# Performance work log

Hardware: AMD Instinct MI355X
Metric: run time of the kernel (lower is better)

The kernel has to match this reference:

```python
import jax, jax.numpy as jnp
import numpy as np
import math

D_MODEL = 1024
NUM_HEADS = 16
B, L = 2, 2048
# scale_level=0, patch_time_span=1 -> effective_stride=1
PERIODS = (1.0, 30.0)
WEIGHTS = (0.8, 0.4)
SIGMAS = (0.5, 2.0)


def setup_inputs() -> dict:
    key = jax.random.key(0)
    ks = jax.random.split(key, 10)
    s = 1.0 / math.sqrt(D_MODEL)
    inp = {
        "x": jax.random.normal(ks[0], (B, L, D_MODEL), dtype=jnp.float32),
        "Wq": jax.random.normal(ks[1], (D_MODEL, D_MODEL), dtype=jnp.float32) * s,
        "bq": jax.random.normal(ks[2], (D_MODEL,), dtype=jnp.float32) * 0.01,
        "Wk": jax.random.normal(ks[3], (D_MODEL, D_MODEL), dtype=jnp.float32) * s,
        "bk": jax.random.normal(ks[4], (D_MODEL,), dtype=jnp.float32) * 0.01,
        "Wv": jax.random.normal(ks[5], (D_MODEL, D_MODEL), dtype=jnp.float32) * s,
        "bv": jax.random.normal(ks[6], (D_MODEL,), dtype=jnp.float32) * 0.01,
        "Wo": jax.random.normal(ks[7], (D_MODEL, D_MODEL), dtype=jnp.float32) * s,
        "bo": jax.random.normal(ks[8], (D_MODEL,), dtype=jnp.float32) * 0.01,
        "prior_lambda": jnp.asarray(2.0, dtype=jnp.float32),
    }
    return inp


def _gaussian_mask(length):
    idx = jnp.arange(length, dtype=jnp.float32)
    delta = jnp.abs(idx[:, None] - idx[None, :])  # [L, L]
    mask = jnp.zeros_like(delta)
    for p, w, sigma in zip(PERIODS, WEIGHTS, SIGMAS):
        if p < 0.2:
            continue
        mask = mask + w * jnp.exp(-((delta - p) ** 2) / (2.0 * sigma ** 2))
    return mask


def reference(x, Wq, bq, Wk, bk, Wv, bv, Wo, bo, prior_lambda):
    Bx, Lx, D = x.shape
    H = NUM_HEADS
    hd = D // H

    def split_heads(t):  # [B, L, D] -> [B, H, L, hd]
        return t.reshape(Bx, Lx, H, hd).transpose(0, 2, 1, 3)

    Q = split_heads(x @ Wq.T + bq)
    K = split_heads(x @ Wk.T + bk)
    V = split_heads(x @ Wv.T + bv)

    scores = jnp.einsum("bhqd,bhkd->bhqk", Q, K) / math.sqrt(hd)
    scores = scores + prior_lambda * _gaussian_mask(Lx)[None, None, :, :]
    attn = jax.nn.softmax(scores, axis=-1)
    out = jnp.einsum("bhqk,bhkd->bhqd", attn, V)
    out = out.transpose(0, 2, 1, 3).reshape(Bx, Lx, D)
    return out @ Wo.T + bo
```

## Files before the change

### kernel.cpp

```cpp
#include <hip/hip_runtime.h>

#define D_MODEL 1024
#define SEQ_L   2048
#define NHEADS  16
#define HDIM    64
#define NROWS   4096

#define QSCALE 0.18033688011112042f
#define LOG2E  1.4426950408889634f

#if __has_builtin(__builtin_amdgcn_exp2f)
#define EXP2F(x) __builtin_amdgcn_exp2f(x)
#else
#define EXP2F(x) __expf((x) * 0.6931471805599453f)
#endif

typedef __attribute__((ext_vector_type(8))) short short8;
typedef __attribute__((ext_vector_type(4))) short short4v;
typedef __attribute__((ext_vector_type(4))) float floatx4;
typedef __attribute__((ext_vector_type(4))) unsigned short ushort4v;
typedef unsigned short ushort;

static __device__ __forceinline__ ushort f2bf(float f) {
    unsigned int u = __float_as_uint(f);
    u += 0x7FFFu + ((u >> 16) & 1u);
    return (ushort)(u >> 16);
}

static __device__ __forceinline__ floatx4 mfma16(short8 a, short8 b, floatx4 c) {
    return __builtin_amdgcn_mfma_f32_16x16x32_bf16(a, b, c, 0, 0, 0);
}

static __device__ __forceinline__ floatx4 mfma16k16(short4v a, short4v b, floatx4 c) {
    return __builtin_amdgcn_mfma_f32_16x16x16bf16_1k(a, b, c, 0, 0, 0);
}

static __device__ __forceinline__ void store8bf(ushort* dst, float4 a, float4 b) {
    uint4 pk;
    pk.x = (unsigned)f2bf(a.x) | ((unsigned)f2bf(a.y) << 16);
    pk.y = (unsigned)f2bf(a.z) | ((unsigned)f2bf(a.w) << 16);
    pk.z = (unsigned)f2bf(b.x) | ((unsigned)f2bf(b.y) << 16);
    pk.w = (unsigned)f2bf(b.z) | ((unsigned)f2bf(b.w) << 16);
    *(uint4*)dst = pk;
}

static __device__ __forceinline__ void gll16(const ushort* g, ushort* l) {
    __builtin_amdgcn_global_load_lds(
        (const __attribute__((address_space(1))) unsigned int*)(const unsigned int*)g,
        (__attribute__((address_space(3))) unsigned int*)(unsigned int*)l,
        16, 0, 0);
}

__global__ __launch_bounds__(256) void convert_bf16(
    const float* __restrict__ x,
    const float* __restrict__ wq, const float* __restrict__ wk,
    const float* __restrict__ wv, const float* __restrict__ wo,
    ushort* __restrict__ xb, ushort* __restrict__ wb3, ushort* __restrict__ wob)
{
    const int seg = blockIdx.y;
    const float* src;
    ushort* dst;
    int n;
    if      (seg == 0) { src = x;  dst = xb;                n = 4194304; }
    else if (seg == 1) { src = wq; dst = wb3;               n = 1048576; }
    else if (seg == 2) { src = wk; dst = wb3 + 1048576;     n = 1048576; }
    else if (seg == 3) { src = wv; dst = wb3 + 2097152;     n = 1048576; }
    else               { src = wo; dst = wob;               n = 1048576; }
    const int i = (blockIdx.x * 256 + threadIdx.x) * 8;
    if (i >= n) return;
    float4 a = *(const float4*)(src + i);
    float4 b = *(const float4*)(src + i + 4);
    store8bf(dst + i, a, b);
}

__global__ __launch_bounds__(256) void gemm_qkv(
    const ushort* __restrict__ A, const ushort* __restrict__ B,
    const float* __restrict__ bq, const float* __restrict__ bk,
    const float* __restrict__ bv,
    ushort* __restrict__ Qo, ushort* __restrict__ Ko, ushort* __restrict__ Vo)
{
    __shared__ ushort As[128 * 32];
    __shared__ ushort Bs[128 * 32];

    const int tid  = threadIdx.x;
    const int w    = tid >> 6;
    const int lane = tid & 63;
    const int l15  = lane & 15;
    const int quad = lane >> 4;
    const int wm   = w & 1;
    const int wn   = w >> 1;

    const int bm = blockIdx.y * 128;
    const int bn = blockIdx.x * 128;
    const int z  = blockIdx.x >> 3;

    const int r0 = w * 16 + (lane >> 2);
    const int r1 = r0 + 64;
    const int c_ = lane & 3;
    const int g0 = c_ ^ ((r0 >> 1) & 3);
    const int g1 = c_ ^ ((r1 >> 1) & 3);

    const ushort* a0p = A + (size_t)(bm + r0) * 1024 + g0 * 8;
    const ushort* a1p = A + (size_t)(bm + r1) * 1024 + g1 * 8;
    const ushort* b0p = B + (size_t)(bn + r0) * 1024 + g0 * 8;
    const ushort* b1p = B + (size_t)(bn + r1) * 1024 + g1 * 8;
    ushort* lA0 = &As[r0 * 32 + c_ * 8];
    ushort* lA1 = &As[r1 * 32 + c_ * 8];
    ushort* lB0 = &Bs[r0 * 32 + c_ * 8];
    ushort* lB1 = &Bs[r1 * 32 + c_ * 8];

    const int cA = (quad ^ ((l15 >> 1) & 3)) * 8;

    floatx4 acc[4][4];
#pragma unroll
    for (int i = 0; i < 4; i++)
#pragma unroll
        for (int j = 0; j < 4; j++) acc[i][j] = (floatx4){0.f, 0.f, 0.f, 0.f};

    if (z == 2) {
        for (int k0 = 0; k0 < 1024; k0 += 32) {
            __syncthreads();
            gll16(a0p + k0, lA0);
            gll16(a1p + k0, lA1);
            gll16(b0p + k0, lB0);
            gll16(b1p + k0, lB1);
            __syncthreads();

            short8 af[4], bf[4];
#pragma unroll
            for (int mi = 0; mi < 4; mi++)
                af[mi] = *(const short8*)&As[(wm * 64 + mi * 16 + l15) * 32 + cA];
#pragma unroll
            for (int ni = 0; ni < 4; ni++)
                bf[ni] = *(const short8*)&Bs[(wn * 64 + ni * 16 + l15) * 32 + cA];
#pragma unroll
            for (int mi = 0; mi < 4; mi++)
#pragma unroll
                for (int ni = 0; ni < 4; ni++)
                    acc[mi][ni] = mfma16(af[mi], bf[ni], acc[mi][ni]);
        }
#pragma unroll
        for (int ni = 0; ni < 4; ni++) {
            const int col = bn + wn * 64 + ni * 16 + l15;
            const int within = col & 1023;
            const int h  = within >> 6;
            const int hd = within & 63;
            const float bvl = bv[within];
#pragma unroll
            for (int mi = 0; mi < 4; mi++) {
                const int row = bm + wm * 64 + mi * 16 + quad * 4;
                const int bb = row >> 11, li = row & 2047;
                ushort4v pk;
#pragma unroll
                for (int r = 0; r < 4; r++) pk[r] = f2bf(acc[mi][ni][r] + bvl);
                *(ushort4v*)(Vo + ((size_t)(bb * NHEADS + h) * HDIM + hd) * SEQ_L + li) = pk;
            }
        }
    } else {
        for (int k0 = 0; k0 < 1024; k0 += 32) {
            __syncthreads();
            gll16(a0p + k0, lA0);
            gll16(a1p + k0, lA1);
            gll16(b0p + k0, lB0);
            gll16(b1p + k0, lB1);
            __syncthreads();

            short8 af[4], bf[4];
#pragma unroll
            for (int mi = 0; mi < 4; mi++)
                af[mi] = *(const short8*)&As[(wm * 64 + mi * 16 + l15) * 32 + cA];
#pragma unroll
            for (int ni = 0; ni < 4; ni++)
                bf[ni] = *(const short8*)&Bs[(wn * 64 + ni * 16 + l15) * 32 + cA];
#pragma unroll
            for (int mi = 0; mi < 4; mi++)
#pragma unroll
                for (int ni = 0; ni < 4; ni++)
                    acc[mi][ni] = mfma16(bf[ni], af[mi], acc[mi][ni]);
        }
        const float* bias = z ? bk : bq;
        const float scale = z ? 1.0f : QSCALE;
        ushort* outp = z ? Ko : Qo;
        const int cwbase = (bn & 1023) + wn * 64;
        const int h = cwbase >> 6;
#pragma unroll
        for (int ni = 0; ni < 4; ni++) {
            const int hd0 = ni * 16 + quad * 4;
            const float4 bb4 = *(const float4*)&bias[cwbase + hd0];
            const float bv0 = bb4.x, bv1 = bb4.y, bv2 = bb4.z, bv3 = bb4.w;
#pragma unroll
            for (int mi = 0; mi < 4; mi++) {
                const int row = bm + wm * 64 + mi * 16 + l15;
                const int bb = row >> 11, li = row & 2047;
                ushort4v pk;
                pk[0] = f2bf((acc[mi][ni][0] + bv0) * scale);
                pk[1] = f2bf((acc[mi][ni][1] + bv1) * scale);
                pk[2] = f2bf((acc[mi][ni][2] + bv2) * scale);
                pk[3] = f2bf((acc[mi][ni][3] + bv3) * scale);
                *(ushort4v*)(outp + ((size_t)(bb * NHEADS + h) * SEQ_L + li) * HDIM + hd0) = pk;
            }
        }
    }
}

__global__ __launch_bounds__(256, 4) void attn(
    const ushort* __restrict__ Q,
    const ushort* __restrict__ K,
    const ushort* __restrict__ Vt,
    const float* __restrict__ lam,
    ushort* __restrict__ O0, ushort* __restrict__ O1,
    float* __restrict__ Lw)
{
    __shared__ float mtab[128];
    __shared__ ushort Ks[2][64 * 64];
    __shared__ ushort Vts[2][64 * 64];

    const int tid  = threadIdx.x;
    const int wave = tid >> 6;
    const int lane = tid & 63;
    const int l15  = lane & 15;
    const int quad = lane >> 4;

    const int qb = blockIdx.x;
    const int h  = blockIdx.y;
    const int zz = blockIdx.z;
    const int bz = zz >> 1;
    const int sp = zz & 1;
    const int bh = bz * NHEADS + h;
    const int q0 = qb * 128;
    const int kb = sp * 1024;

    const float lambda = *lam;
    if (tid < 128) {
        float d  = (float)tid;
        float e1 = (d - 1.f) * (d - 1.f);
        float e2 = (d - 30.f) * (d - 30.f);
        mtab[tid] = LOG2E * lambda *
                    (0.8f * __expf(-2.0f * e1) + 0.4f * __expf(-0.125f * e2));
    }

    const ushort* qp =
        Q + ((size_t)bh * SEQ_L + q0 + wave * 16 + l15) * HDIM + quad * 8;
    short8 qf[2][2];
    qf[0][0] = *(const short8*)qp;
    qf[0][1] = *(const short8*)(qp + 32);
    qf[1][0] = *(const short8*)(qp + 64 * HDIM);
    qf[1][1] = *(const short8*)(qp + 64 * HDIM + 32);

    const ushort* kbase = K  + ((size_t)bh * SEQ_L) * HDIM;
    const ushort* vbase = Vt + ((size_t)bh * HDIM) * SEQ_L;

    const int cid0 = tid, cid1 = 256 + tid;
    const int row0 = cid0 >> 3, row1 = cid1 >> 3;
    const int cl0  = (cid0 & 7) ^ (row0 & 7);
    const int cl1  = (cid1 & 7) ^ (row1 & 7);
    const ushort* kg0 = kbase + (size_t)(kb + row0) * HDIM + cl0 * 8;
    const ushort* kg1 = kbase + (size_t)(kb + row1) * HDIM + cl1 * 8;
    const ushort* vg0 = vbase + (size_t)row0 * SEQ_L + kb + cl0 * 8;
    const ushort* vg1 = vbase + (size_t)row1 * SEQ_L + kb + cl1 * 8;

    floatx4 o[2][4];
#pragma unroll
    for (int g = 0; g < 2; g++)
#pragma unroll
        for (int i = 0; i < 4; i++) o[g][i] = (floatx4){0.f, 0.f, 0.f, 0.f};
    floatx4 ol[2];
    ol[0] = (floatx4){0.f, 0.f, 0.f, 0.f};
    ol[1] = (floatx4){0.f, 0.f, 0.f, 0.f};

    short4v ones;
    ones[0] = 0x3F80; ones[1] = 0x3F80; ones[2] = 0x3F80; ones[3] = 0x3F80;

    gll16(kg0, &Ks[0][cid0 * 8]);
    gll16(kg1, &Ks[0][cid1 * 8]);
    gll16(vg0, &Vts[0][cid0 * 8]);
    gll16(vg1, &Vts[0][cid1 * 8]);

    const int xo = l15 & 7;

    for (int t = 0; t < 16; t++) {
        const int cur = t & 1;
        __syncthreads();
        if (t + 1 < 16) {
            const int nxt = cur ^ 1;
            const int koff = (t + 1) * 64;
            gll16(kg0 + (size_t)koff * HDIM, &Ks[nxt][cid0 * 8]);
            gll16(kg1 + (size_t)koff * HDIM, &Ks[nxt][cid1 * 8]);
            gll16(vg0 + koff, &Vts[nxt][cid0 * 8]);
            gll16(vg1 + koff, &Vts[nxt][cid1 * 8]);
        }

        floatx4 s[2][4];
#pragma unroll
        for (int g = 0; g < 2; g++)
#pragma unroll
            for (int i = 0; i < 4; i++) s[g][i] = (floatx4){0.f, 0.f, 0.f, 0.f};
#pragma unroll
        for (int kk = 0; kk < 2; kk++) {
#pragma unroll
            for (int nt = 0; nt < 4; nt++) {
                const int slot = (kk * 4 + quad) ^ xo;
                short8 kf = *(const short8*)&Ks[cur][(nt * 16 + l15) * 64 + slot * 8];
                s[0][nt] = mfma16(kf, qf[0][kk], s[0][nt]);
                s[1][nt] = mfma16(kf, qf[1][kk], s[1][nt]);
            }
        }

        const int j = sp * 16 + t;
#pragma unroll
        for (int g = 0; g < 2; g++) {
            const int tg = j - (qb * 2 + g);
            if (tg >= -1 && tg <= 1) {
                const int qg = q0 + g * 64 + wave * 16 + l15;
#pragma unroll
                for (int nt = 0; nt < 4; nt++) {
                    const int kgi = j * 64 + nt * 16 + quad * 4;
#pragma unroll
                    for (int r = 0; r < 4; r++) {
                        int dq = qg - (kgi + r);
                        int ad = dq < 0 ? -dq : dq;
                        s[g][nt][r] += mtab[ad];
                    }
                }
            }
        }

        short4v pb[2][4];
#pragma unroll
        for (int g = 0; g < 2; g++) {
#pragma unroll
            for (int nt = 0; nt < 4; nt++) {
                unsigned ur[4];
#pragma unroll
                for (int r = 0; r < 4; r++)
                    ur[r] = __float_as_uint(EXP2F(s[g][nt][r])) + 0x8000u;
                uint2 pk;
                pk.x = __builtin_amdgcn_perm(ur[1], ur[0], 0x07060302u);
                pk.y = __builtin_amdgcn_perm(ur[3], ur[2], 0x07060302u);
                pb[g][nt] = __builtin_bit_cast(short4v, pk);
            }
        }

#pragma unroll
        for (int kc = 0; kc < 4; kc++) {
#pragma unroll
            for (int nt = 0; nt < 4; nt++) {
                const int slot = (2 * kc + (quad >> 1)) ^ xo;
                short4v vf = *(const short4v*)
                    &Vts[cur][(nt * 16 + l15) * 64 + slot * 8 + (quad & 1) * 4];
                o[0][nt] = mfma16k16(vf, pb[0][kc], o[0][nt]);
                o[1][nt] = mfma16k16(vf, pb[1][kc], o[1][nt]);
            }
            ol[0] = mfma16k16(ones, pb[0][kc], ol[0]);
            ol[1] = mfma16k16(ones, pb[1][kc], ol[1]);
        }
    }

    ushort* Osp = sp ? O1 : O0;
#pragma unroll
    for (int g = 0; g < 2; g++) {
        const int qg = q0 + g * 64 + wave * 16 + l15;
        if (quad == 0)
            Lw[((size_t)(sp * 2 + bz) * NHEADS + h) * SEQ_L + qg] = ol[g][0];
        ushort* obase = Osp + ((size_t)bz * SEQ_L + qg) * D_MODEL + h * HDIM;
#pragma unroll
        for (int nt = 0; nt < 4; nt++) {
            ushort4v pk;
#pragma unroll
            for (int r = 0; r < 4; r++) pk[r] = f2bf(o[g][nt][r]);
            *(ushort4v*)(obase + nt * 16 + quad * 4) = pk;
        }
    }
}

__global__ __launch_bounds__(256) void merge_attn(
    const ushort* __restrict__ O0, const ushort* __restrict__ O1,
    const float* __restrict__ Lw, ushort* __restrict__ Aout)
{
    const int gid = blockIdx.x * 256 + threadIdx.x;
    const int i = gid * 8;
    const int row = i >> 10;
    const int h   = (i >> 6) & 15;
    const int bz  = row >> 11, q = row & 2047;
    const int li  = (bz * NHEADS + h) * SEQ_L + q;
    const float linv = 1.f / (Lw[li] + Lw[2 * NHEADS * SEQ_L + li]);

    uint4 a = *(const uint4*)(O0 + i);
    uint4 b = *(const uint4*)(O1 + i);
    unsigned aw[4] = {a.x, a.y, a.z, a.w};
    unsigned bw[4] = {b.x, b.y, b.z, b.w};
    uint4 res;
    unsigned rw[4];
#pragma unroll
    for (int k = 0; k < 4; k++) {
        float alo = __uint_as_float(aw[k] << 16);
        float ahi = __uint_as_float(aw[k] & 0xFFFF0000u);
        float blo = __uint_as_float(bw[k] << 16);
        float bhi = __uint_as_float(bw[k] & 0xFFFF0000u);
        float lo = (alo + blo) * linv;
        float hi = (ahi + bhi) * linv;
        rw[k] = (unsigned)f2bf(lo) | ((unsigned)f2bf(hi) << 16);
    }
    res.x = rw[0]; res.y = rw[1]; res.z = rw[2]; res.w = rw[3];
    *(uint4*)(Aout + i) = res;
}

__global__ __launch_bounds__(256) void gemm_out(
    const ushort* __restrict__ A, const ushort* __restrict__ B,
    const float* __restrict__ bo, float* __restrict__ out)
{
    __shared__ ushort As[64 * 32];
    __shared__ ushort Bs[128 * 32];

    const int tid  = threadIdx.x;
    const int w    = tid >> 6;
    const int lane = tid & 63;
    const int l15  = lane & 15;
    const int quad = lane >> 4;

    const int bm = blockIdx.y * 64;
    const int bn = blockIdx.x * 128;

    const int r0 = w * 16 + (lane >> 2);
    const int r1 = r0 + 64;
    const int c_ = lane & 3;
    const int g0 = c_ ^ ((r0 >> 1) & 3);
    const int g1 = c_ ^ ((r1 >> 1) & 3);

    const ushort* a0p = A + (size_t)(bm + r0) * 1024 + g0 * 8;
    const ushort* b0p = B + (size_t)(bn + r0) * 1024 + g0 * 8;
    const ushort* b1p = B + (size_t)(bn + r1) * 1024 + g1 * 8;
    ushort* lA0 = &As[r0 * 32 + c_ * 8];
    ushort* lB0 = &Bs[r0 * 32 + c_ * 8];
    ushort* lB1 = &Bs[r1 * 32 + c_ * 8];

    const int cA = (quad ^ ((l15 >> 1) & 3)) * 8;

    floatx4 acc[4][2];
#pragma unroll
    for (int i = 0; i < 4; i++)
#pragma unroll
        for (int j = 0; j < 2; j++) acc[i][j] = (floatx4){0.f, 0.f, 0.f, 0.f};

    for (int k0 = 0; k0 < 1024; k0 += 32) {
        __syncthreads();
        gll16(a0p + k0, lA0);
        gll16(b0p + k0, lB0);
        gll16(b1p + k0, lB1);
        __syncthreads();

        short8 af[4], bf[2];
#pragma unroll
        for (int mi = 0; mi < 4; mi++)
            af[mi] = *(const short8*)&As[(mi * 16 + l15) * 32 + cA];
#pragma unroll
        for (int ni = 0; ni < 2; ni++)
            bf[ni] = *(const short8*)&Bs[(w * 32 + ni * 16 + l15) * 32 + cA];
#pragma unroll
        for (int mi = 0; mi < 4; mi++)
#pragma unroll
            for (int ni = 0; ni < 2; ni++)
                acc[mi][ni] = mfma16(bf[ni], af[mi], acc[mi][ni]);
    }

#pragma unroll
    for (int ni = 0; ni < 2; ni++) {
        const int col0 = bn + w * 32 + ni * 16 + quad * 4;
        const float4 bb4 = *(const float4*)&bo[col0];
#pragma unroll
        for (int mi = 0; mi < 4; mi++) {
            const int row = bm + mi * 16 + l15;
            float4 st;
            st.x = acc[mi][ni][0] + bb4.x;
            st.y = acc[mi][ni][1] + bb4.y;
            st.z = acc[mi][ni][2] + bb4.z;
            st.w = acc[mi][ni][3] + bb4.w;
            *(float4*)(out + (size_t)row * 1024 + col0) = st;
        }
    }
}

extern "C" void kernel_launch(void* const* d_in, const int* in_sizes, int n_in,
                              void* d_out, int out_size, void* d_ws, size_t ws_size,
                              hipStream_t stream)
{
    const float* x   = (const float*)d_in[0];
    const float* Wq  = (const float*)d_in[1];
    const float* bq  = (const float*)d_in[2];
    const float* Wk  = (const float*)d_in[3];
    const float* bk  = (const float*)d_in[4];
    const float* Wv  = (const float*)d_in[5];
    const float* bv  = (const float*)d_in[6];
    const float* Wo  = (const float*)d_in[7];
    const float* bo  = (const float*)d_in[8];
    const float* lam = (const float*)d_in[9];
    float* out = (float*)d_out;

    const size_t NELEM = (size_t)NROWS * D_MODEL;
    ushort* Qw  = (ushort*)d_ws;
    ushort* Kw  = Qw + NELEM;
    ushort* Vw  = Kw + NELEM;
    ushort* O0  = Vw + NELEM;
    ushort* O1  = O0 + NELEM;
    ushort* XA  = O1 + NELEM;
    ushort* Wb3 = XA + NELEM;
    ushort* Wob = Wb3 + 3 * 1024 * 1024;
    float*  Lw  = (float*)(Wob + 1024 * 1024);

    dim3 gc(2048, 5);
    convert_bf16<<<gc, 256, 0, stream>>>(x, Wq, Wk, Wv, Wo, XA, Wb3, Wob);

    dim3 g1(3072 / 128, NROWS / 128);
    gemm_qkv<<<g1, 256, 0, stream>>>(XA, Wb3, bq, bk, bv, Qw, Kw, Vw);

    dim3 g2(SEQ_L / 128, NHEADS, 4);
    attn<<<g2, 256, 0, stream>>>(Qw, Kw, Vw, lam, O0, O1, Lw);

    merge_attn<<<NELEM / (256 * 8), 256, 0, stream>>>(O0, O1, Lw, XA);

    dim3 g3(1024 / 128, NROWS / 64);
    gemm_out<<<g3, 256, 0, stream>>>(XA, Wob, bo, out);
}
```

Baseline: 210.2 us.

## Double-buffer LDS tiles in QKV and output projection GEMMs

```diff
diff --git a/kernel.cpp b/kernel.cpp
--- a/kernel.cpp
+++ b/kernel.cpp
@@ -79,8 +79,8 @@
     const float* __restrict__ bv,
     ushort* __restrict__ Qo, ushort* __restrict__ Ko, ushort* __restrict__ Vo)
 {
-    __shared__ ushort As[128 * 32];
-    __shared__ ushort Bs[128 * 32];
+    __shared__ ushort As[2][128 * 32];
+    __shared__ ushort Bs[2][128 * 32];
 
     const int tid  = threadIdx.x;
     const int w    = tid >> 6;
@@ -104,10 +104,8 @@
     const ushort* a1p = A + (size_t)(bm + r1) * 1024 + g1 * 8;
     const ushort* b0p = B + (size_t)(bn + r0) * 1024 + g0 * 8;
     const ushort* b1p = B + (size_t)(bn + r1) * 1024 + g1 * 8;
-    ushort* lA0 = &As[r0 * 32 + c_ * 8];
-    ushort* lA1 = &As[r1 * 32 + c_ * 8];
-    ushort* lB0 = &Bs[r0 * 32 + c_ * 8];
-    ushort* lB1 = &Bs[r1 * 32 + c_ * 8];
+    const int sA0 = r0 * 32 + c_ * 8;
+    const int sA1 = r1 * 32 + c_ * 8;
 
     const int cA = (quad ^ ((l15 >> 1) & 3)) * 8;
 
@@ -117,28 +115,46 @@
 #pragma unroll
         for (int j = 0; j < 4; j++) acc[i][j] = (floatx4){0.f, 0.f, 0.f, 0.f};
 
-    if (z == 2) {
-        for (int k0 = 0; k0 < 1024; k0 += 32) {
-            __syncthreads();
-            gll16(a0p + k0, lA0);
-            gll16(a1p + k0, lA1);
-            gll16(b0p + k0, lB0);
-            gll16(b1p + k0, lB1);
-            __syncthreads();
-
-            short8 af[4], bf[4];
-#pragma unroll
-            for (int mi = 0; mi < 4; mi++)
-                af[mi] = *(const short8*)&As[(wm * 64 + mi * 16 + l15) * 32 + cA];
-#pragma unroll
-            for (int ni = 0; ni < 4; ni++)
-                bf[ni] = *(const short8*)&Bs[(wn * 64 + ni * 16 + l15) * 32 + cA];
+    gll16(a0p, &As[0][sA0]);
+    gll16(a1p, &As[0][sA1]);
+    gll16(b0p, &Bs[0][sA0]);
+    gll16(b1p, &Bs[0][sA1]);
+
+    for (int it = 0; it < 32; it++) {
+        const int cur = it & 1;
+        __syncthreads();
+        if (it + 1 < 32) {
+            const int k0 = (it + 1) * 32;
+            const int nxt = cur ^ 1;
+            gll16(a0p + k0, &As[nxt][sA0]);
+            gll16(a1p + k0, &As[nxt][sA1]);
+            gll16(b0p + k0, &Bs[nxt][sA0]);
+            gll16(b1p + k0, &Bs[nxt][sA1]);
+        }
+
+        short8 af[4], bf[4];
+#pragma unroll
+        for (int mi = 0; mi < 4; mi++)
+            af[mi] = *(const short8*)&As[cur][(wm * 64 + mi * 16 + l15) * 32 + cA];
+#pragma unroll
+        for (int ni = 0; ni < 4; ni++)
+            bf[ni] = *(const short8*)&Bs[cur][(wn * 64 + ni * 16 + l15) * 32 + cA];
+        if (z == 2) {
 #pragma unroll
             for (int mi = 0; mi < 4; mi++)
 #pragma unroll
                 for (int ni = 0; ni < 4; ni++)
                     acc[mi][ni] = mfma16(af[mi], bf[ni], acc[mi][ni]);
-        }
+        } else {
+#pragma unroll
+            for (int mi = 0; mi < 4; mi++)
+#pragma unroll
+                for (int ni = 0; ni < 4; ni++)
+                    acc[mi][ni] = mfma16(bf[ni], af[mi], acc[mi][ni]);
+        }
+    }
+
+    if (z == 2) {
 #pragma unroll
         for (int ni = 0; ni < 4; ni++) {
             const int col = bn + wn * 64 + ni * 16 + l15;
@@ -157,27 +173,6 @@
             }
         }
     } else {
-        for (int k0 = 0; k0 < 1024; k0 += 32) {
-            __syncthreads();
-            gll16(a0p + k0, lA0);
-            gll16(a1p + k0, lA1);
-            gll16(b0p + k0, lB0);
-            gll16(b1p + k0, lB1);
-            __syncthreads();
-
-            short8 af[4], bf[4];
-#pragma unroll
-            for (int mi = 0; mi < 4; mi++)
-                af[mi] = *(const short8*)&As[(wm * 64 + mi * 16 + l15) * 32 + cA];
-#pragma unroll
-            for (int ni = 0; ni < 4; ni++)
-                bf[ni] = *(const short8*)&Bs[(wn * 64 + ni * 16 + l15) * 32 + cA];
-#pragma unroll
-            for (int mi = 0; mi < 4; mi++)
-#pragma unroll
-                for (int ni = 0; ni < 4; ni++)
-                    acc[mi][ni] = mfma16(bf[ni], af[mi], acc[mi][ni]);
-        }
         const float* bias = z ? bk : bq;
         const float scale = z ? 1.0f : QSCALE;
         ushort* outp = z ? Ko : Qo;
@@ -187,16 +182,15 @@
         for (int ni = 0; ni < 4; ni++) {
             const int hd0 = ni * 16 + quad * 4;
             const float4 bb4 = *(const float4*)&bias[cwbase + hd0];
-            const float bv0 = bb4.x, bv1 = bb4.y, bv2 = bb4.z, bv3 = bb4.w;
 #pragma unroll
             for (int mi = 0; mi < 4; mi++) {
                 const int row = bm + wm * 64 + mi * 16 + l15;
                 const int bb = row >> 11, li = row & 2047;
                 ushort4v pk;
-                pk[0] = f2bf((acc[mi][ni][0] + bv0) * scale);
-                pk[1] = f2bf((acc[mi][ni][1] + bv1) * scale);
-                pk[2] = f2bf((acc[mi][ni][2] + bv2) * scale);
-                pk[3] = f2bf((acc[mi][ni][3] + bv3) * scale);
+                pk[0] = f2bf((acc[mi][ni][0] + bb4.x) * scale);
+                pk[1] = f2bf((acc[mi][ni][1] + bb4.y) * scale);
+                pk[2] = f2bf((acc[mi][ni][2] + bb4.z) * scale);
+                pk[3] = f2bf((acc[mi][ni][3] + bb4.w) * scale);
                 *(ushort4v*)(outp + ((size_t)(bb * NHEADS + h) * SEQ_L + li) * HDIM + hd0) = pk;
             }
         }
@@ -409,8 +403,8 @@
     const ushort* __restrict__ A, const ushort* __restrict__ B,
     const float* __restrict__ bo, float* __restrict__ out)
 {
-    __shared__ ushort As[64 * 32];
-    __shared__ ushort Bs[128 * 32];
+    __shared__ ushort As[2][64 * 32];
+    __shared__ ushort Bs[2][128 * 32];
 
     const int tid  = threadIdx.x;
     const int w    = tid >> 6;
@@ -430,9 +424,8 @@
     const ushort* a0p = A + (size_t)(bm + r0) * 1024 + g0 * 8;
     const ushort* b0p = B + (size_t)(bn + r0) * 1024 + g0 * 8;
     const ushort* b1p = B + (size_t)(bn + r1) * 1024 + g1 * 8;
-    ushort* lA0 = &As[r0 * 32 + c_ * 8];
-    ushort* lB0 = &Bs[r0 * 32 + c_ * 8];
-    ushort* lB1 = &Bs[r1 * 32 + c_ * 8];
+    const int sA0 = r0 * 32 + c_ * 8;
+    const int sA1 = r1 * 32 + c_ * 8;
 
     const int cA = (quad ^ ((l15 >> 1) & 3)) * 8;
 
@@ -442,20 +435,28 @@
 #pragma unroll
         for (int j = 0; j < 2; j++) acc[i][j] = (floatx4){0.f, 0.f, 0.f, 0.f};
 
-    for (int k0 = 0; k0 < 1024; k0 += 32) {
+    gll16(a0p, &As[0][sA0]);
+    gll16(b0p, &Bs[0][sA0]);
+    gll16(b1p, &Bs[0][sA1]);
+
+    for (int it = 0; it < 32; it++) {
+        const int cur = it & 1;
         __syncthreads();
-        gll16(a0p + k0, lA0);
-        gll16(b0p + k0, lB0);
-        gll16(b1p + k0, lB1);
-        __syncthreads();
+        if (it + 1 < 32) {
+            const int k0 = (it + 1) * 32;
+            const int nxt = cur ^ 1;
+            gll16(a0p + k0, &As[nxt][sA0]);
+            gll16(b0p + k0, &Bs[nxt][sA0]);
+            gll16(b1p + k0, &Bs[nxt][sA1]);
+        }
 
         short8 af[4], bf[2];
 #pragma unroll
         for (int mi = 0; mi < 4; mi++)
-            af[mi] = *(const short8*)&As[(mi * 16 + l15) * 32 + cA];
+            af[mi] = *(const short8*)&As[cur][(mi * 16 + l15) * 32 + cA];
 #pragma unroll
         for (int ni = 0; ni < 2; ni++)
-            bf[ni] = *(const short8*)&Bs[(w * 32 + ni * 16 + l15) * 32 + cA];
+            bf[ni] = *(const short8*)&Bs[cur][(w * 32 + ni * 16 + l15) * 32 + cA];
 #pragma unroll
         for (int mi = 0; mi < 4; mi++)
 #pragma unroll
```

Result: slower. 226.6 us (+7.8%).
